# Kernel tuning notes

Hardware: AMD Instinct MI355X
Metric: run time of the kernel (lower is better)

Reference implementation:

```python
import jax, jax.numpy as jnp
import numpy as np

N = 100000
IN_CH = 256
HID = 64
OUT_CH = 40
E1 = 1_600_000
E2 = 3_200_000


def spmm(rows, cols, vals, x, n):
    # out[r] = sum over edges e with rows[e]==r of vals[e] * x[cols[e]]
    return jax.ops.segment_sum(vals[:, None] * x[cols], rows, num_segments=n)


def setup_inputs() -> dict:
    key = jax.random.key(0)
    ks = jax.random.split(key, 12)
    x = jax.random.normal(ks[0], (N, IN_CH), dtype=jnp.float32)
    edge_index = jax.random.randint(ks[1], (2, E1), 0, N, dtype=jnp.int32)
    adj_src = jax.random.randint(ks[2], (E1,), 0, N, dtype=jnp.int32)
    adj_dst = jax.random.randint(ks[3], (E1,), 0, N, dtype=jnp.int32)
    adj_val = jax.random.uniform(ks[4], (E1,), dtype=jnp.float32)
    adj2_src = jax.random.randint(ks[5], (E2,), 0, N, dtype=jnp.int32)
    adj2_dst = jax.random.randint(ks[6], (E2,), 0, N, dtype=jnp.int32)
    adj2_val = jax.random.uniform(ks[7], (E2,), dtype=jnp.float32)
    fc1_w = jax.random.normal(ks[8], (HID, IN_CH), dtype=jnp.float32) * (1.0 / np.sqrt(IN_CH))
    fc_out_w = jax.random.normal(ks[9], (OUT_CH, 3 * HID), dtype=jnp.float32) * (1.0 / np.sqrt(3 * HID))
    fc_out_b = jax.random.normal(ks[10], (OUT_CH,), dtype=jnp.float32) * 0.01
    return {"x": x, "edge_index": edge_index,
            "adj_src": adj_src, "adj_dst": adj_dst, "adj_val": adj_val,
            "adj2_src": adj2_src, "adj2_dst": adj2_dst, "adj2_val": adj2_val,
            "fc1_w": fc1_w, "fc_out_w": fc_out_w, "fc_out_b": fc_out_b}


def reference(x, edge_index, adj_src, adj_dst, adj_val,
              adj2_src, adj2_dst, adj2_val, fc1_w, fc_out_w, fc_out_b):
    # h0 = fc1(x), no bias
    h0 = x @ fc1_w.T                                  # [N, HID]
    # num_layers = 1: one round of 1-hop and 2-hop propagation
    h1 = spmm(adj_src, adj_dst, adj_val, h0, N)       # [N, HID]
    h2 = spmm(adj2_src, adj2_dst, adj2_val, h0, N)    # [N, HID]
    h = jnp.concatenate([h0, h1, h2], axis=1)         # [N, 3*HID]
    # dropout is identity in eval mode
    return h @ fc_out_w.T + fc_out_b                  # [N, OUT_CH]
```

## Files before the change

kernel.cpp:

```cpp
#include <hip/hip_runtime.h>

#define Nn 100000
#define INC 256
#define OC 40
#define GEL 4000000u
#define NB 782
#define CAP 7040
#define CHUNK 4096
#define OVFCAP 65536
#define BSTRIDE 264

#define MP_OFF   0
#define G_OFF    131072
#define GCUR_OFF 16131072
#define OVFC_OFF (GCUR_OFF + 3128)
#define OVFL_OFF (OVFC_OFF + 8)
#define PAY_OFF  (OVFL_OFF + OVFCAP*12)

typedef __attribute__((ext_vector_type(8))) short bf16x8;
typedef __attribute__((ext_vector_type(4))) float f32x4;

__device__ __forceinline__ unsigned short f2bf(float f) {
    unsigned b = __float_as_uint(f);
    b += 0x7FFFu + ((b >> 16) & 1u);
    return (unsigned short)(b >> 16);
}
__device__ __forceinline__ float bf2f(unsigned short u) {
    return __uint_as_float(((unsigned)u) << 16);
}

__global__ void make_M(const float* __restrict__ fc1_w,
                       const float* __restrict__ fc_out_w,
                       unsigned short* __restrict__ Mb) {
    int j = blockIdx.x;
    int k = threadIdx.x;
    float acc = 0.f;
    if (j < 120) {
        int i = j / 40, o = j - i * 40;
        const float* wrow = fc_out_w + o * 192 + i * 64;
#pragma unroll 8
        for (int t = 0; t < 64; ++t)
            acc = fmaf(wrow[t], fc1_w[t * 256 + k], acc);
    }
    Mb[j * 256 + k] = (j < 120) ? f2bf(acc) : (unsigned short)0;
}

__global__ __launch_bounds__(256, 2) void gemm_mfma(
    const float* __restrict__ x, const unsigned short* __restrict__ Mb,
    const float* __restrict__ bias, float* __restrict__ out,
    unsigned short* __restrict__ g) {
    __shared__ unsigned short mlds[120 * BSTRIDE];
    const int tid = threadIdx.x;
    const int w = tid >> 6;
    const int l = tid & 63;
    const int lane15 = l & 15;
    const int quad = l >> 4;

    for (int i = tid; i < 3840; i += 256) {
        int r = i >> 5;
        int k8 = (i & 31) * 8;
        uint4 v = *(const uint4*)(Mb + r * 256 + k8);
        *(uint4*)(mlds + r * BSTRIDE + k8) = v;
    }
    __syncthreads();

    const int arow = blockIdx.x * 64 + w * 16 + lane15;
    const bool rok = arow < Nn;
    const float* xp = x + (size_t)arow * INC + quad * 8;

    f32x4 acc[8];
#pragma unroll
    for (int c = 0; c < 8; ++c) acc[c] = (f32x4){0.f, 0.f, 0.f, 0.f};

    float4 c0 = make_float4(0, 0, 0, 0), c1 = make_float4(0, 0, 0, 0);
    if (rok) { c0 = *(const float4*)(xp); c1 = *(const float4*)(xp + 4); }

#pragma unroll
    for (int kt = 0; kt < 8; ++kt) {
        float4 n0 = make_float4(0, 0, 0, 0), n1 = make_float4(0, 0, 0, 0);
        if (kt < 7 && rok) {
            n0 = *(const float4*)(xp + (kt + 1) * 32);
            n1 = *(const float4*)(xp + (kt + 1) * 32 + 4);
        }
        bf16x8 af;
        af[0] = (short)f2bf(c0.x); af[1] = (short)f2bf(c0.y);
        af[2] = (short)f2bf(c0.z); af[3] = (short)f2bf(c0.w);
        af[4] = (short)f2bf(c1.x); af[5] = (short)f2bf(c1.y);
        af[6] = (short)f2bf(c1.z); af[7] = (short)f2bf(c1.w);
        const unsigned short* bbase = mlds + kt * 32 + quad * 8 + lane15 * BSTRIDE;
#pragma unroll
        for (int ct = 0; ct < 8; ++ct) {
            if (ct * 16 >= 120) break;
            bf16x8 bf = *(const bf16x8*)(bbase + ct * 16 * BSTRIDE);
            acc[ct] = __builtin_amdgcn_mfma_f32_16x16x32_bf16(af, bf, acc[ct], 0, 0, 0);
        }
        c0 = n0; c1 = n1;
    }

#pragma unroll
    for (int ct = 0; ct < 8; ++ct) {
        int col = ct * 16 + lane15;
        if (col >= 120) continue;
        int ib = col / 40;
        int cc = col - ib * 40;
        float badd = (ib == 0) ? bias[cc] : 0.f;
#pragma unroll
        for (int reg = 0; reg < 4; ++reg) {
            int gr = blockIdx.x * 64 + w * 16 + quad * 4 + reg;
            if (gr >= Nn) continue;
            float v = acc[ct][reg] + badd;
            if (ib == 0) out[gr * 40 + cc] = v;
            else g[(unsigned)(ib - 1) * GEL + (unsigned)gr * 40u + cc] = f2bf(v);
        }
    }
}

__global__ __launch_bounds__(512) void partition(
    const int* __restrict__ s1, const int* __restrict__ d1, const float* __restrict__ v1, int E1,
    const int* __restrict__ s2, const int* __restrict__ d2, const float* __restrict__ v2, int E2,
    int* __restrict__ gcur, uint2* __restrict__ payload,
    int* __restrict__ ovf_cnt, unsigned* __restrict__ ovf) {
    __shared__ int cnt[NB];
    __shared__ int loff[NB + 1];
    __shared__ int scanbuf[512];
    __shared__ int gbase[NB];
    __shared__ int lcur[NB];
    __shared__ uint2 pay[CHUNK];
    __shared__ int dest[CHUNK];

    const int t = threadIdx.x;
    const int Etot = E1 + E2;
    const int e0 = blockIdx.x * CHUNK;

    for (int i = t; i < NB; i += 512) cnt[i] = 0;
    __syncthreads();

    int my_s[8]; unsigned my_p[8]; float my_v[8]; bool my_ok[8];
#pragma unroll
    for (int j = 0; j < 8; ++j) {
        int e = e0 + j * 512 + t;
        my_ok[j] = (e < Etot);
        if (my_ok[j]) {
            int s, d; float v; unsigned gbit;
            if (e < E1) { s = s1[e]; d = d1[e]; v = v1[e]; gbit = 0u; }
            else { int e2 = e - E1; s = s2[e2]; d = d2[e2]; v = v2[e2]; gbit = 1u; }
            my_s[j] = s;
            my_p[j] = (unsigned)d | (gbit << 17) | (((unsigned)s & 127u) << 18);
            my_v[j] = v;
            atomicAdd(&cnt[s >> 7], 1);
        }
    }
    __syncthreads();

    int b0 = t * 2;
    int c0 = (b0 < NB) ? cnt[b0] : 0;
    int c1 = (b0 + 1 < NB) ? cnt[b0 + 1] : 0;
    scanbuf[t] = c0 + c1;
    __syncthreads();
    for (int off = 1; off < 512; off <<= 1) {
        int v = (t >= off) ? scanbuf[t - off] : 0;
        __syncthreads();
        scanbuf[t] += v;
        __syncthreads();
    }
    int ebase = scanbuf[t] - (c0 + c1);
    if (b0 < NB) loff[b0] = ebase;
    if (b0 + 1 < NB) loff[b0 + 1] = ebase + c0;
    if (t == 511) loff[NB] = scanbuf[511];
    __syncthreads();

    for (int i = t; i < NB; i += 512) {
        int c = cnt[i];
        gbase[i] = c ? atomicAdd(&gcur[i], c) : 0;
        lcur[i] = loff[i];
    }
    __syncthreads();

#pragma unroll
    for (int j = 0; j < 8; ++j) {
        if (my_ok[j]) {
            int b = my_s[j] >> 7;
            int lp = atomicAdd(&lcur[b], 1);
            pay[lp] = make_uint2(my_p[j], __float_as_uint(my_v[j]));
            int go = gbase[b] + (lp - loff[b]);
            if (go < CAP) dest[lp] = b * CAP + go;
            else {
                dest[lp] = -1;
                int op = atomicAdd(ovf_cnt, 1);
                if (op < OVFCAP) {
                    ovf[3 * op] = (unsigned)my_s[j];
                    ovf[3 * op + 1] = my_p[j];
                    ovf[3 * op + 2] = __float_as_uint(my_v[j]);
                }
            }
        }
    }
    __syncthreads();

    int tot = loff[NB];
    for (int i = t; i < tot; i += 512) {
        int dd = dest[i];
        if (dd >= 0) payload[dd] = pay[i];
    }
}

__global__ __launch_bounds__(640, 7) void bucket_gather(
    const int* __restrict__ gcur, const uint2* __restrict__ payload,
    const unsigned short* __restrict__ g, float* __restrict__ out) {
    __shared__ unsigned spay[CAP];
    __shared__ int cnt[128];
    __shared__ int rs[129];
    __shared__ int cur[128];
    __shared__ int sb[128];

    const int t = threadIdx.x;
    const int b = blockIdx.x;
    int n = gcur[b];
    n = (n < CAP) ? n : CAP;

    if (t < 128) cnt[t] = 0;
    __syncthreads();

    const uint2* pb = payload + (size_t)b * CAP;
    const unsigned* pbx = (const unsigned*)pb;
    for (int i = t; i < n; i += 640)
        atomicAdd(&cnt[(pbx[2 * i] >> 18) & 127u], 1);
    __syncthreads();

    if (t < 128) sb[t] = cnt[t];
    __syncthreads();
    for (int off = 1; off < 128; off <<= 1) {
        int v = 0;
        if (t < 128 && t >= off) v = sb[t - off];
        __syncthreads();
        if (t < 128) sb[t] += v;
        __syncthreads();
    }
    if (t < 128) { int e = sb[t] - cnt[t]; rs[t] = e; cur[t] = e; }
    if (t == 0) rs[128] = n;
    __syncthreads();

    for (int i = t; i < n; i += 640) {
        uint2 p = pb[i];
        unsigned q = (unsigned)(__uint_as_float(p.y) * 16383.f + 0.5f);
        int pos = atomicAdd(&cur[(p.x >> 18) & 127u], 1);
        spay[pos] = (p.x & 0x3FFFFu) | (q << 18);
    }
    __syncthreads();

    const int le = t / 10;
    const int q4 = (t - le * 10) * 4;
    const float VS = 1.0f / 16383.0f;
#pragma unroll
    for (int pass = 0; pass < 2; ++pass) {
        int row = pass * 64 + le;
        int e0 = rs[row], e1 = rs[row + 1];
        float4 a0 = make_float4(0.f, 0.f, 0.f, 0.f);
        float4 a1 = make_float4(0.f, 0.f, 0.f, 0.f);
        int e = e0;
        for (; e + 4 <= e1; e += 4) {
            unsigned p0 = spay[e], p1 = spay[e + 1], p2 = spay[e + 2], p3 = spay[e + 3];
            ushort4 u0 = *(const ushort4*)(g + (p0 & 0x1FFFFu) * 40u + ((p0 >> 17) & 1u) * GEL + q4);
            ushort4 u1 = *(const ushort4*)(g + (p1 & 0x1FFFFu) * 40u + ((p1 >> 17) & 1u) * GEL + q4);
            ushort4 u2 = *(const ushort4*)(g + (p2 & 0x1FFFFu) * 40u + ((p2 >> 17) & 1u) * GEL + q4);
            ushort4 u3 = *(const ushort4*)(g + (p3 & 0x1FFFFu) * 40u + ((p3 >> 17) & 1u) * GEL + q4);
            float v0 = (float)(p0 >> 18) * VS, v1 = (float)(p1 >> 18) * VS;
            float v2 = (float)(p2 >> 18) * VS, v3 = (float)(p3 >> 18) * VS;
            a0.x = fmaf(v0, bf2f(u0.x), a0.x); a0.y = fmaf(v0, bf2f(u0.y), a0.y);
            a0.z = fmaf(v0, bf2f(u0.z), a0.z); a0.w = fmaf(v0, bf2f(u0.w), a0.w);
            a1.x = fmaf(v1, bf2f(u1.x), a1.x); a1.y = fmaf(v1, bf2f(u1.y), a1.y);
            a1.z = fmaf(v1, bf2f(u1.z), a1.z); a1.w = fmaf(v1, bf2f(u1.w), a1.w);
            a0.x = fmaf(v2, bf2f(u2.x), a0.x); a0.y = fmaf(v2, bf2f(u2.y), a0.y);
            a0.z = fmaf(v2, bf2f(u2.z), a0.z); a0.w = fmaf(v2, bf2f(u2.w), a0.w);
            a1.x = fmaf(v3, bf2f(u3.x), a1.x); a1.y = fmaf(v3, bf2f(u3.y), a1.y);
            a1.z = fmaf(v3, bf2f(u3.z), a1.z); a1.w = fmaf(v3, bf2f(u3.w), a1.w);
        }
        for (; e < e1; ++e) {
            unsigned p = spay[e];
            float v = (float)(p >> 18) * VS;
            ushort4 u = *(const ushort4*)(g + (p & 0x1FFFFu) * 40u + ((p >> 17) & 1u) * GEL + q4);
            a0.x = fmaf(v, bf2f(u.x), a0.x); a0.y = fmaf(v, bf2f(u.y), a0.y);
            a0.z = fmaf(v, bf2f(u.z), a0.z); a0.w = fmaf(v, bf2f(u.w), a0.w);
        }
        int gr = b * 128 + row;
        if (gr < Nn && e1 > e0) {
            float* po = out + gr * 40 + q4;
            float4 o = *(float4*)po;
            o.x += a0.x + a1.x; o.y += a0.y + a1.y;
            o.z += a0.z + a1.z; o.w += a0.w + a1.w;
            *(float4*)po = o;
        }
    }
}

__global__ __launch_bounds__(256) void ovf_scatter(
    const int* __restrict__ ovf_cnt, const unsigned* __restrict__ ovf,
    const unsigned short* __restrict__ g, float* __restrict__ out) {
    int n = *ovf_cnt;
    n = (n < OVFCAP) ? n : OVFCAP;
    int total = n * 40;
    for (int i = blockIdx.x * 256 + threadIdx.x; i < total; i += 2048) {
        int idx = i / 40, c = i % 40;
        unsigned s = ovf[3 * idx];
        unsigned p = ovf[3 * idx + 1];
        float v = __uint_as_float(ovf[3 * idx + 2]);
        unsigned dst = p & 0x1FFFFu;
        unsigned gph = (p >> 17) & 1u;
        float gf = bf2f(g[gph * GEL + dst * 40 + c]);
        unsafeAtomicAdd(out + s * 40 + c, v * gf);
    }
}

extern "C" void kernel_launch(void* const* d_in, const int* in_sizes, int n_in,
                              void* d_out, int out_size, void* d_ws, size_t ws_size,
                              hipStream_t stream) {
    const float* x        = (const float*)d_in[0];
    const int*   adj_src  = (const int*)d_in[2];
    const int*   adj_dst  = (const int*)d_in[3];
    const float* adj_val  = (const float*)d_in[4];
    const int*   adj2_src = (const int*)d_in[5];
    const int*   adj2_dst = (const int*)d_in[6];
    const float* adj2_val = (const float*)d_in[7];
    const float* fc1_w    = (const float*)d_in[8];
    const float* fc_out_w = (const float*)d_in[9];
    const float* fc_out_b = (const float*)d_in[10];
    float* out = (float*)d_out;

    char* ws = (char*)d_ws;
    unsigned short* Mb      = (unsigned short*)(ws + MP_OFF);
    unsigned short* g       = (unsigned short*)(ws + G_OFF);
    int*            gcur    = (int*)(ws + GCUR_OFF);
    int*            ovf_cnt = (int*)(ws + OVFC_OFF);
    unsigned*       ovf     = (unsigned*)(ws + OVFL_OFF);
    uint2*          payload = (uint2*)(ws + PAY_OFF);

    const int E1 = in_sizes[2];
    const int E2 = in_sizes[5];
    const int Etot = E1 + E2;

    make_M<<<128, 256, 0, stream>>>(fc1_w, fc_out_w, Mb);
    gemm_mfma<<<(Nn + 63) / 64, 256, 0, stream>>>(x, Mb, fc_out_b, out, g);

    hipMemsetAsync(gcur, 0, NB * sizeof(int) + 16, stream);
    partition<<<(Etot + CHUNK - 1) / CHUNK, 512, 0, stream>>>(
        adj_src, adj_dst, adj_val, E1, adj2_src, adj2_dst, adj2_val, E2,
        gcur, payload, ovf_cnt, ovf);
    bucket_gather<<<NB, 640, 0, stream>>>(gcur, payload, g, out);
    ovf_scatter<<<8, 256, 0, stream>>>(ovf_cnt, ovf, g, out);
}
```

Baseline: 407.3 us.

## Retune GEMM blocking, streamline edge partition, split bucket gather into halves

The GEMM now runs 512-thread blocks over 128 rows and prefetches x two k-steps ahead through a 3-deep register ring. Partition moves to 1024 threads, reuses the local atomic rank as the slot position instead of a second atomic pass, and computes global destinations in the write-out loop using a 16-bit bucket id. Bucket gather launches two blocks per bucket, each handling 64 rows with a smaller LDS buffer, which raises block count and occupancy. Rows that overflow the half-buffer fall back to per-element global atomics. The larger blocks and extra filtering pass over each bucket's payload add cost in exchange.

Measured after the change: 395.4 us. -2.9%, faster.

```diff
diff --git a/kernel.cpp b/kernel.cpp
--- a/kernel.cpp
+++ b/kernel.cpp
@@ -6,6 +6,7 @@
 #define GEL 4000000u
 #define NB 782
 #define CAP 7040
+#define CAPH 3744
 #define CHUNK 4096
 #define OVFCAP 65536
 #define BSTRIDE 264
@@ -45,7 +46,7 @@
     Mb[j * 256 + k] = (j < 120) ? f2bf(acc) : (unsigned short)0;
 }
 
-__global__ __launch_bounds__(256, 2) void gemm_mfma(
+__global__ __launch_bounds__(512, 4) void gemm_mfma(
     const float* __restrict__ x, const unsigned short* __restrict__ Mb,
     const float* __restrict__ bias, float* __restrict__ out,
     unsigned short* __restrict__ g) {
@@ -56,7 +57,7 @@
     const int lane15 = l & 15;
     const int quad = l >> 4;
 
-    for (int i = tid; i < 3840; i += 256) {
+    for (int i = tid; i < 3840; i += 512) {
         int r = i >> 5;
         int k8 = (i & 31) * 8;
         uint4 v = *(const uint4*)(Mb + r * 256 + k8);
@@ -64,7 +65,7 @@
     }
     __syncthreads();
 
-    const int arow = blockIdx.x * 64 + w * 16 + lane15;
+    const int arow = blockIdx.x * 128 + w * 16 + lane15;
     const bool rok = arow < Nn;
     const float* xp = x + (size_t)arow * INC + quad * 8;
 
@@ -72,21 +73,29 @@
 #pragma unroll
     for (int c = 0; c < 8; ++c) acc[c] = (f32x4){0.f, 0.f, 0.f, 0.f};
 
-    float4 c0 = make_float4(0, 0, 0, 0), c1 = make_float4(0, 0, 0, 0);
-    if (rok) { c0 = *(const float4*)(xp); c1 = *(const float4*)(xp + 4); }
+    float4 pa[3], pb_[3];
+#pragma unroll
+    for (int p = 0; p < 2; ++p) {
+        pa[p] = make_float4(0, 0, 0, 0); pb_[p] = make_float4(0, 0, 0, 0);
+        if (rok) { pa[p] = *(const float4*)(xp + p * 32); pb_[p] = *(const float4*)(xp + p * 32 + 4); }
+    }
 
 #pragma unroll
     for (int kt = 0; kt < 8; ++kt) {
-        float4 n0 = make_float4(0, 0, 0, 0), n1 = make_float4(0, 0, 0, 0);
-        if (kt < 7 && rok) {
-            n0 = *(const float4*)(xp + (kt + 1) * 32);
-            n1 = *(const float4*)(xp + (kt + 1) * 32 + 4);
-        }
+        const int nb = (kt + 2) % 3;
+        if (kt + 2 < 8) {
+            pa[nb] = make_float4(0, 0, 0, 0); pb_[nb] = make_float4(0, 0, 0, 0);
+            if (rok) {
+                pa[nb] = *(const float4*)(xp + (kt + 2) * 32);
+                pb_[nb] = *(const float4*)(xp + (kt + 2) * 32 + 4);
+            }
+        }
+        const int cu = kt % 3;
         bf16x8 af;
-        af[0] = (short)f2bf(c0.x); af[1] = (short)f2bf(c0.y);
-        af[2] = (short)f2bf(c0.z); af[3] = (short)f2bf(c0.w);
-        af[4] = (short)f2bf(c1.x); af[5] = (short)f2bf(c1.y);
-        af[6] = (short)f2bf(c1.z); af[7] = (short)f2bf(c1.w);
+        af[0] = (short)f2bf(pa[cu].x); af[1] = (short)f2bf(pa[cu].y);
+        af[2] = (short)f2bf(pa[cu].z); af[3] = (short)f2bf(pa[cu].w);
+        af[4] = (short)f2bf(pb_[cu].x); af[5] = (short)f2bf(pb_[cu].y);
+        af[6] = (short)f2bf(pb_[cu].z); af[7] = (short)f2bf(pb_[cu].w);
         const unsigned short* bbase = mlds + kt * 32 + quad * 8 + lane15 * BSTRIDE;
 #pragma unroll
         for (int ct = 0; ct < 8; ++ct) {
@@ -94,7 +103,6 @@
             bf16x8 bf = *(const bf16x8*)(bbase + ct * 16 * BSTRIDE);
             acc[ct] = __builtin_amdgcn_mfma_f32_16x16x32_bf16(af, bf, acc[ct], 0, 0, 0);
         }
-        c0 = n0; c1 = n1;
     }
 
 #pragma unroll
@@ -106,7 +114,7 @@
         float badd = (ib == 0) ? bias[cc] : 0.f;
 #pragma unroll
         for (int reg = 0; reg < 4; ++reg) {
-            int gr = blockIdx.x * 64 + w * 16 + quad * 4 + reg;
+            int gr = blockIdx.x * 128 + w * 16 + quad * 4 + reg;
             if (gr >= Nn) continue;
             float v = acc[ct][reg] + badd;
             if (ib == 0) out[gr * 40 + cc] = v;
@@ -115,181 +123,186 @@
     }
 }
 
-__global__ __launch_bounds__(512) void partition(
+__global__ __launch_bounds__(1024, 8) void partition(
     const int* __restrict__ s1, const int* __restrict__ d1, const float* __restrict__ v1, int E1,
     const int* __restrict__ s2, const int* __restrict__ d2, const float* __restrict__ v2, int E2,
     int* __restrict__ gcur, uint2* __restrict__ payload,
     int* __restrict__ ovf_cnt, unsigned* __restrict__ ovf) {
     __shared__ int cnt[NB];
     __shared__ int loff[NB + 1];
-    __shared__ int scanbuf[512];
     __shared__ int gbase[NB];
-    __shared__ int lcur[NB];
+    __shared__ int scanbuf[1024];
     __shared__ uint2 pay[CHUNK];
-    __shared__ int dest[CHUNK];
+    __shared__ unsigned short dest16[CHUNK];
 
     const int t = threadIdx.x;
     const int Etot = E1 + E2;
     const int e0 = blockIdx.x * CHUNK;
 
-    for (int i = t; i < NB; i += 512) cnt[i] = 0;
-    __syncthreads();
-
-    int my_s[8]; unsigned my_p[8]; float my_v[8]; bool my_ok[8];
-#pragma unroll
-    for (int j = 0; j < 8; ++j) {
-        int e = e0 + j * 512 + t;
+    for (int i = t; i < NB; i += 1024) cnt[i] = 0;
+    __syncthreads();
+
+    int my_b[4]; int my_rank[4]; unsigned my_p[4]; float my_v[4]; bool my_ok[4];
+#pragma unroll
+    for (int j = 0; j < 4; ++j) {
+        int e = e0 + j * 1024 + t;
         my_ok[j] = (e < Etot);
         if (my_ok[j]) {
             int s, d; float v; unsigned gbit;
             if (e < E1) { s = s1[e]; d = d1[e]; v = v1[e]; gbit = 0u; }
             else { int e2 = e - E1; s = s2[e2]; d = d2[e2]; v = v2[e2]; gbit = 1u; }
-            my_s[j] = s;
+            my_b[j] = s >> 7;
             my_p[j] = (unsigned)d | (gbit << 17) | (((unsigned)s & 127u) << 18);
             my_v[j] = v;
-            atomicAdd(&cnt[s >> 7], 1);
-        }
-    }
-    __syncthreads();
-
-    int b0 = t * 2;
-    int c0 = (b0 < NB) ? cnt[b0] : 0;
-    int c1 = (b0 + 1 < NB) ? cnt[b0 + 1] : 0;
-    scanbuf[t] = c0 + c1;
-    __syncthreads();
-    for (int off = 1; off < 512; off <<= 1) {
+            my_rank[j] = atomicAdd(&cnt[my_b[j]], 1);
+        }
+    }
+    __syncthreads();
+
+    int c = (t < NB) ? cnt[t] : 0;
+    scanbuf[t] = c;
+    __syncthreads();
+    for (int off = 1; off < 1024; off <<= 1) {
         int v = (t >= off) ? scanbuf[t - off] : 0;
         __syncthreads();
         scanbuf[t] += v;
         __syncthreads();
     }
-    int ebase = scanbuf[t] - (c0 + c1);
-    if (b0 < NB) loff[b0] = ebase;
-    if (b0 + 1 < NB) loff[b0 + 1] = ebase + c0;
-    if (t == 511) loff[NB] = scanbuf[511];
-    __syncthreads();
-
-    for (int i = t; i < NB; i += 512) {
-        int c = cnt[i];
-        gbase[i] = c ? atomicAdd(&gcur[i], c) : 0;
-        lcur[i] = loff[i];
-    }
-    __syncthreads();
-
-#pragma unroll
-    for (int j = 0; j < 8; ++j) {
+    if (t < NB) loff[t] = scanbuf[t] - c;
+    if (t == 1023) loff[NB] = scanbuf[1023];
+    __syncthreads();
+
+    if (t < NB) {
+        int cc = cnt[t];
+        gbase[t] = cc ? atomicAdd(&gcur[t], cc) : 0;
+    }
+    __syncthreads();
+
+#pragma unroll
+    for (int j = 0; j < 4; ++j) {
         if (my_ok[j]) {
-            int b = my_s[j] >> 7;
-            int lp = atomicAdd(&lcur[b], 1);
+            int lp = loff[my_b[j]] + my_rank[j];
             pay[lp] = make_uint2(my_p[j], __float_as_uint(my_v[j]));
-            int go = gbase[b] + (lp - loff[b]);
-            if (go < CAP) dest[lp] = b * CAP + go;
-            else {
-                dest[lp] = -1;
-                int op = atomicAdd(ovf_cnt, 1);
-                if (op < OVFCAP) {
-                    ovf[3 * op] = (unsigned)my_s[j];
-                    ovf[3 * op + 1] = my_p[j];
-                    ovf[3 * op + 2] = __float_as_uint(my_v[j]);
-                }
+            dest16[lp] = (unsigned short)my_b[j];
+        }
+    }
+    __syncthreads();
+
+    int tot = loff[NB];
+    for (int i = t; i < tot; i += 1024) {
+        int b = dest16[i];
+        int go = gbase[b] + (i - loff[b]);
+        if (go < CAP) payload[(size_t)b * CAP + go] = pay[i];
+        else {
+            int op = atomicAdd(ovf_cnt, 1);
+            if (op < OVFCAP) {
+                unsigned px = pay[i].x;
+                ovf[3 * op] = ((unsigned)b << 7) | ((px >> 18) & 127u);
+                ovf[3 * op + 1] = px;
+                ovf[3 * op + 2] = pay[i].y;
             }
         }
-    }
-    __syncthreads();
-
-    int tot = loff[NB];
-    for (int i = t; i < tot; i += 512) {
-        int dd = dest[i];
-        if (dd >= 0) payload[dd] = pay[i];
     }
 }
 
 __global__ __launch_bounds__(640, 7) void bucket_gather(
     const int* __restrict__ gcur, const uint2* __restrict__ payload,
     const unsigned short* __restrict__ g, float* __restrict__ out) {
-    __shared__ unsigned spay[CAP];
-    __shared__ int cnt[128];
-    __shared__ int rs[129];
-    __shared__ int cur[128];
-    __shared__ int sb[128];
+    __shared__ unsigned spay[CAPH];
+    __shared__ int cnt[64];
+    __shared__ int rs[65];
+    __shared__ int cur[64];
+    __shared__ int sb[64];
 
     const int t = threadIdx.x;
-    const int b = blockIdx.x;
+    const int b = blockIdx.x >> 1;
+    const unsigned h = blockIdx.x & 1;
     int n = gcur[b];
     n = (n < CAP) ? n : CAP;
 
-    if (t < 128) cnt[t] = 0;
+    if (t < 64) cnt[t] = 0;
     __syncthreads();
 
     const uint2* pb = payload + (size_t)b * CAP;
     const unsigned* pbx = (const unsigned*)pb;
-    for (int i = t; i < n; i += 640)
-        atomicAdd(&cnt[(pbx[2 * i] >> 18) & 127u], 1);
-    __syncthreads();
-
-    if (t < 128) sb[t] = cnt[t];
-    __syncthreads();
-    for (int off = 1; off < 128; off <<= 1) {
+    for (int i = t; i < n; i += 640) {
+        unsigned r = (pbx[2 * i] >> 18) & 127u;
+        if ((r >> 6) == h) atomicAdd(&cnt[r & 63u], 1);
+    }
+    __syncthreads();
+
+    if (t < 64) sb[t] = cnt[t];
+    __syncthreads();
+    for (int off = 1; off < 64; off <<= 1) {
         int v = 0;
-        if (t < 128 && t >= off) v = sb[t - off];
+        if (t < 64 && t >= off) v = sb[t - off];
         __syncthreads();
-        if (t < 128) sb[t] += v;
+        if (t < 64) sb[t] += v;
         __syncthreads();
     }
-    if (t < 128) { int e = sb[t] - cnt[t]; rs[t] = e; cur[t] = e; }
-    if (t == 0) rs[128] = n;
+    if (t < 64) { int e = sb[t] - cnt[t]; rs[t] = e; cur[t] = e; }
+    if (t == 0) rs[64] = 0;
+    __syncthreads();
+    if (t == 63) rs[64] = sb[63];
     __syncthreads();
 
     for (int i = t; i < n; i += 640) {
         uint2 p = pb[i];
-        unsigned q = (unsigned)(__uint_as_float(p.y) * 16383.f + 0.5f);
-        int pos = atomicAdd(&cur[(p.x >> 18) & 127u], 1);
-        spay[pos] = (p.x & 0x3FFFFu) | (q << 18);
+        unsigned r = (p.x >> 18) & 127u;
+        if ((r >> 6) == h) {
+            unsigned q = (unsigned)(__uint_as_float(p.y) * 16383.f + 0.5f);
+            int pos = atomicAdd(&cur[r & 63u], 1);
+            if (pos < CAPH) spay[pos] = (p.x & 0x3FFFFu) | (q << 18);
+            else {
+                unsigned s = ((unsigned)b << 7) | r;
+                unsigned base = (p.x & 0x1FFFFu) * 40u + ((p.x >> 17) & 1u) * GEL;
+                float v = __uint_as_float(p.y);
+                for (int cch = 0; cch < 40; ++cch)
+                    unsafeAtomicAdd(out + s * 40 + cch, v * bf2f(g[base + cch]));
+            }
+        }
     }
     __syncthreads();
 
     const int le = t / 10;
     const int q4 = (t - le * 10) * 4;
     const float VS = 1.0f / 16383.0f;
-#pragma unroll
-    for (int pass = 0; pass < 2; ++pass) {
-        int row = pass * 64 + le;
-        int e0 = rs[row], e1 = rs[row + 1];
-        float4 a0 = make_float4(0.f, 0.f, 0.f, 0.f);
-        float4 a1 = make_float4(0.f, 0.f, 0.f, 0.f);
-        int e = e0;
-        for (; e + 4 <= e1; e += 4) {
-            unsigned p0 = spay[e], p1 = spay[e + 1], p2 = spay[e + 2], p3 = spay[e + 3];
-            ushort4 u0 = *(const ushort4*)(g + (p0 & 0x1FFFFu) * 40u + ((p0 >> 17) & 1u) * GEL + q4);
-            ushort4 u1 = *(const ushort4*)(g + (p1 & 0x1FFFFu) * 40u + ((p1 >> 17) & 1u) * GEL + q4);
-            ushort4 u2 = *(const ushort4*)(g + (p2 & 0x1FFFFu) * 40u + ((p2 >> 17) & 1u) * GEL + q4);
-            ushort4 u3 = *(const ushort4*)(g + (p3 & 0x1FFFFu) * 40u + ((p3 >> 17) & 1u) * GEL + q4);
-            float v0 = (float)(p0 >> 18) * VS, v1 = (float)(p1 >> 18) * VS;
-            float v2 = (float)(p2 >> 18) * VS, v3 = (float)(p3 >> 18) * VS;
-            a0.x = fmaf(v0, bf2f(u0.x), a0.x); a0.y = fmaf(v0, bf2f(u0.y), a0.y);
-            a0.z = fmaf(v0, bf2f(u0.z), a0.z); a0.w = fmaf(v0, bf2f(u0.w), a0.w);
-            a1.x = fmaf(v1, bf2f(u1.x), a1.x); a1.y = fmaf(v1, bf2f(u1.y), a1.y);
-            a1.z = fmaf(v1, bf2f(u1.z), a1.z); a1.w = fmaf(v1, bf2f(u1.w), a1.w);
-            a0.x = fmaf(v2, bf2f(u2.x), a0.x); a0.y = fmaf(v2, bf2f(u2.y), a0.y);
-            a0.z = fmaf(v2, bf2f(u2.z), a0.z); a0.w = fmaf(v2, bf2f(u2.w), a0.w);
-            a1.x = fmaf(v3, bf2f(u3.x), a1.x); a1.y = fmaf(v3, bf2f(u3.y), a1.y);
-            a1.z = fmaf(v3, bf2f(u3.z), a1.z); a1.w = fmaf(v3, bf2f(u3.w), a1.w);
-        }
-        for (; e < e1; ++e) {
-            unsigned p = spay[e];
-            float v = (float)(p >> 18) * VS;
-            ushort4 u = *(const ushort4*)(g + (p & 0x1FFFFu) * 40u + ((p >> 17) & 1u) * GEL + q4);
-            a0.x = fmaf(v, bf2f(u.x), a0.x); a0.y = fmaf(v, bf2f(u.y), a0.y);
-            a0.z = fmaf(v, bf2f(u.z), a0.z); a0.w = fmaf(v, bf2f(u.w), a0.w);
-        }
-        int gr = b * 128 + row;
-        if (gr < Nn && e1 > e0) {
-            float* po = out + gr * 40 + q4;
-            float4 o = *(float4*)po;
-            o.x += a0.x + a1.x; o.y += a0.y + a1.y;
-            o.z += a0.z + a1.z; o.w += a0.w + a1.w;
-            *(float4*)po = o;
-        }
+    int e0 = rs[le], e1 = rs[le + 1];
+    e1 = (e1 < CAPH) ? e1 : CAPH;
+    float4 a0 = make_float4(0.f, 0.f, 0.f, 0.f);
+    float4 a1 = make_float4(0.f, 0.f, 0.f, 0.f);
+    int e = e0;
+    for (; e + 4 <= e1; e += 4) {
+        unsigned p0 = spay[e], p1 = spay[e + 1], p2 = spay[e + 2], p3 = spay[e + 3];
+        ushort4 u0 = *(const ushort4*)(g + (p0 & 0x1FFFFu) * 40u + ((p0 >> 17) & 1u) * GEL + q4);
+        ushort4 u1 = *(const ushort4*)(g + (p1 & 0x1FFFFu) * 40u + ((p1 >> 17) & 1u) * GEL + q4);
+        ushort4 u2 = *(const ushort4*)(g + (p2 & 0x1FFFFu) * 40u + ((p2 >> 17) & 1u) * GEL + q4);
+        ushort4 u3 = *(const ushort4*)(g + (p3 & 0x1FFFFu) * 40u + ((p3 >> 17) & 1u) * GEL + q4);
+        float v0 = (float)(p0 >> 18) * VS, v1 = (float)(p1 >> 18) * VS;
+        float v2 = (float)(p2 >> 18) * VS, v3 = (float)(p3 >> 18) * VS;
+        a0.x = fmaf(v0, bf2f(u0.x), a0.x); a0.y = fmaf(v0, bf2f(u0.y), a0.y);
+        a0.z = fmaf(v0, bf2f(u0.z), a0.z); a0.w = fmaf(v0, bf2f(u0.w), a0.w);
+        a1.x = fmaf(v1, bf2f(u1.x), a1.x); a1.y = fmaf(v1, bf2f(u1.y), a1.y);
+        a1.z = fmaf(v1, bf2f(u1.z), a1.z); a1.w = fmaf(v1, bf2f(u1.w), a1.w);
+        a0.x = fmaf(v2, bf2f(u2.x), a0.x); a0.y = fmaf(v2, bf2f(u2.y), a0.y);
+        a0.z = fmaf(v2, bf2f(u2.z), a0.z); a0.w = fmaf(v2, bf2f(u2.w), a0.w);
+        a1.x = fmaf(v3, bf2f(u3.x), a1.x); a1.y = fmaf(v3, bf2f(u3.y), a1.y);
+        a1.z = fmaf(v3, bf2f(u3.z), a1.z); a1.w = fmaf(v3, bf2f(u3.w), a1.w);
+    }
+    for (; e < e1; ++e) {
+        unsigned p = spay[e];
+        float v = (float)(p >> 18) * VS;
+        ushort4 u = *(const ushort4*)(g + (p & 0x1FFFFu) * 40u + ((p >> 17) & 1u) * GEL + q4);
+        a0.x = fmaf(v, bf2f(u.x), a0.x); a0.y = fmaf(v, bf2f(u.y), a0.y);
+        a0.z = fmaf(v, bf2f(u.z), a0.z); a0.w = fmaf(v, bf2f(u.w), a0.w);
+    }
+    int gr = b * 128 + h * 64 + le;
+    if (gr < Nn && e1 > e0) {
+        float* po = out + gr * 40 + q4;
+        float4 o = *(float4*)po;
+        o.x += a0.x + a1.x; o.y += a0.y + a1.y;
+        o.z += a0.z + a1.z; o.w += a0.w + a1.w;
+        *(float4*)po = o;
     }
 }
 
@@ -339,12 +352,12 @@
     const int Etot = E1 + E2;
 
     make_M<<<128, 256, 0, stream>>>(fc1_w, fc_out_w, Mb);
-    gemm_mfma<<<(Nn + 63) / 64, 256, 0, stream>>>(x, Mb, fc_out_b, out, g);
+    gemm_mfma<<<(Nn + 127) / 128, 512, 0, stream>>>(x, Mb, fc_out_b, out, g);
 
     hipMemsetAsync(gcur, 0, NB * sizeof(int) + 16, stream);
-    partition<<<(Etot + CHUNK - 1) / CHUNK, 512, 0, stream>>>(
+    partition<<<(Etot + CHUNK - 1) / CHUNK, 1024, 0, stream>>>(
         adj_src, adj_dst, adj_val, E1, adj2_src, adj2_dst, adj2_val, E2,
         gcur, payload, ovf_cnt, ovf);
-    bucket_gather<<<NB, 640, 0, stream>>>(gcur, payload, g, out);
+    bucket_gather<<<NB * 2, 640, 0, stream>>>(gcur, payload, g, out);
     ovf_scatter<<<8, 256, 0, stream>>>(ovf_cnt, ovf, g, out);
 }
```
